# Kernel tuning notes

Hardware: AMD Instinct MI355X
Metric: run time of the kernel (lower is better)

The kernel has to match this reference:

```python
import jax, jax.numpy as jnp
import numpy as np

T, V, D, L, H, F, R = 1024, 17, 1024, 2, 16, 4096, 32
DH = D // H
LORA_SCALE = 2.0  # lora_alpha / r = 64 / 32
MASK_ID = 16
NEG = jnp.float32(-1e9)


def setup_inputs() -> dict:
    key = jax.random.key(0)
    ks = iter(jax.random.split(key, 64))
    def p(shape, std):
        return jax.random.normal(next(ks), shape, jnp.float32) * std
    inp = {
        "packed_context": jax.random.randint(next(ks), (T,), 0, V),
        "cu_seq_lens": jnp.sort(jax.random.randint(next(ks), (5,), 0, T)),
        "max_seq_len": T,
        "row_coords": jax.random.randint(next(ks), (T,), 0, 64),
        "col_coords": jax.random.randint(next(ks), (T,), 0, 64),
        "num_diffusion_steps": 2,
        "E": p((V, D), 0.02),  # embed rows actually used: weight[:vocab_size]
    }
    shapes = {"q": (D, D), "k": (D, D), "v": (D, D), "o": (D, D),
              "g": (D, F), "u": (D, F), "d": (F, D)}
    for nm, (di, do) in shapes.items():
        inp["W" + nm] = p((L, di, do), di ** -0.5)  # frozen NF4 base weight (dequantized)
        inp["A" + nm] = p((L, di, R), di ** -0.5)   # LoRA A
        inp["B" + nm] = p((L, R, do), 0.01)          # LoRA B (nonzero for grad testing)
    inp["ln1"] = jnp.ones((L, D), jnp.float32)
    inp["ln2"] = jnp.ones((L, D), jnp.float32)
    inp["lnf"] = jnp.ones((D,), jnp.float32)
    return inp


def _rms(x, w):
    return x * jax.lax.rsqrt(jnp.mean(x * x, axis=-1, keepdims=True) + 1e-6) * w


def _lora(x, W, A, B):
    # fused base matmul + low-rank LoRA delta
    return x @ W + LORA_SCALE * ((x @ A) @ B)


def _denoise_step(soft, E, Wq, Aq, Bq, Wk, Ak, Bk, Wv, Av, Bv, Wo, Ao, Bo,
                  Wg, Ag, Bg, Wu, Au, Bu, Wd, Ad, Bd, ln1, ln2, lnf, causal_bias):
    # soft-token embedding: [T,V] @ [V,D]
    x = soft @ E
    inv_sqrt_dh = jnp.float32(1.0 / np.sqrt(DH))
    for l in range(L):
        h = _rms(x, ln1[l])
        q = _lora(h, Wq[l], Aq[l], Bq[l]).reshape(T, H, DH)
        k = _lora(h, Wk[l], Ak[l], Bk[l]).reshape(T, H, DH)
        v = _lora(h, Wv[l], Av[l], Bv[l]).reshape(T, H, DH)
        scores = jnp.einsum('qhd,khd->hqk', q, k) * inv_sqrt_dh + causal_bias
        att = jax.nn.softmax(scores, axis=-1)
        ctx = jnp.einsum('hqk,khd->qhd', att, v).reshape(T, D)
        x = x + _lora(ctx, Wo[l], Ao[l], Bo[l])
        h2 = _rms(x, ln2[l])
        ff = jax.nn.silu(_lora(h2, Wg[l], Ag[l], Bg[l])) * _lora(h2, Wu[l], Au[l], Bu[l])
        x = x + _lora(ff, Wd[l], Ad[l], Bd[l])
    logits = _rms(x, lnf) @ E.T  # tied head over the 17-token task vocab
    return jax.nn.softmax(logits, axis=-1)


def reference(packed_context, cu_seq_lens, max_seq_len, row_coords, col_coords,
              num_diffusion_steps, E, Wq, Aq, Bq, Wk, Ak, Bk, Wv, Av, Bv,
              Wo, Ao, Bo, Wg, Ag, Bg, Wu, Au, Bu, Wd, Ad, Bd, ln1, ln2, lnf):
    causal_bias = jnp.where(jnp.tril(jnp.ones((T, T), bool)), jnp.float32(0.0), NEG)
    is_prompt = (packed_context != MASK_ID)[:, None]  # [T,1]
    ctx_onehot = jax.nn.one_hot(packed_context, V, dtype=jnp.float32)
    soft = jnp.zeros((T, V), jnp.float32).at[:, MASK_ID].set(1.0)
    for _ in range(int(num_diffusion_steps)):
        refined = _denoise_step(soft, E, Wq, Aq, Bq, Wk, Ak, Bk, Wv, Av, Bv,
                                Wo, Ao, Bo, Wg, Ag, Bg, Wu, Au, Bu, Wd, Ad, Bd,
                                ln1, ln2, lnf, causal_bias)
        soft = jnp.where(is_prompt, ctx_onehot, refined)
    return jnp.argmax(soft, axis=-1)
```

## Files before the change

### kernel.cpp

```cpp
#include <hip/hip_runtime.h>
#include <hip/hip_bf16.h>

#define T_LEN 1024
#define D_DIM 1024
#define V_DIM 17
#define H_NUM 16
#define DH_DIM 64
#define F_DIM 4096
#define R_LORA 32
#define N_LAYERS 2
#define N_STEPS 2
#define MASK_ID 16
#define LORA_SCALE 2.0f

typedef __attribute__((ext_vector_type(8))) short bfx8;
typedef __attribute__((ext_vector_type(4))) float f32x4;

typedef unsigned short ushort_t;
typedef unsigned int uint_t;

#define AS1 __attribute__((address_space(1)))
#define AS3 __attribute__((address_space(3)))

__device__ __forceinline__ void gload16(const ushort_t* g, ushort_t* l) {
    __builtin_amdgcn_global_load_lds((const AS1 void*)(const void*)g,
                                     (AS3 void*)(void*)l, 16, 0, 0);
}

__device__ __forceinline__ ushort_t f2bf(float v) {
    __hip_bfloat16 h = __float2bfloat16(v);
    return __builtin_bit_cast(unsigned short, h);
}
__device__ __forceinline__ float bf2f(ushort_t u) {
    return __uint_as_float(((uint_t)u) << 16);
}
__device__ __forceinline__ void split4_store(float y0, float y1, float y2, float y3,
                                             ushort_t* __restrict__ hi, ushort_t* __restrict__ lo,
                                             size_t idx) {
    ushort_t h0 = f2bf(y0), h1 = f2bf(y1), h2 = f2bf(y2), h3 = f2bf(y3);
    ushort_t l0 = f2bf(y0 - bf2f(h0));
    ushort_t l1 = f2bf(y1 - bf2f(h1));
    ushort_t l2 = f2bf(y2 - bf2f(h2));
    ushort_t l3 = f2bf(y3 - bf2f(h3));
    uint2 hv, lv;
    hv.x = (uint_t)h0 | ((uint_t)h1 << 16);
    hv.y = (uint_t)h2 | ((uint_t)h3 << 16);
    lv.x = (uint_t)l0 | ((uint_t)l1 << 16);
    lv.y = (uint_t)l2 | ((uint_t)l3 << 16);
    *(uint2*)(hi + idx) = hv;
    *(uint2*)(lo + idx) = lv;
}

__global__ void init_soft_kernel(float* __restrict__ soft) {
    int idx = blockIdx.x * blockDim.x + threadIdx.x;
    if (idx < T_LEN * V_DIM) {
        soft[idx] = ((idx % V_DIM) == MASK_ID) ? 1.0f : 0.0f;
    }
}

__global__ __launch_bounds__(256) void embed_rms_split_kernel(
    const float* __restrict__ soft, const float* __restrict__ E,
    const float* __restrict__ w, float* __restrict__ x,
    ushort_t* __restrict__ hi, ushort_t* __restrict__ lo)
{
    const int t = blockIdx.x, tid = threadIdx.x;
    __shared__ float srow[V_DIM];
    __shared__ float red[4];
    if (tid < V_DIM) srow[tid] = soft[t * V_DIM + tid];
    __syncthreads();
    const int d0 = tid * 4;
    float4 acc = {0.f, 0.f, 0.f, 0.f};
    #pragma unroll
    for (int v = 0; v < V_DIM; v++) {
        float s = srow[v];
        float4 e = *(const float4*)(E + (size_t)v * D_DIM + d0);
        acc.x = fmaf(s, e.x, acc.x);
        acc.y = fmaf(s, e.y, acc.y);
        acc.z = fmaf(s, e.z, acc.z);
        acc.w = fmaf(s, e.w, acc.w);
    }
    size_t base = (size_t)t * D_DIM + d0;
    *(float4*)(x + base) = acc;
    float ss = acc.x * acc.x + acc.y * acc.y + acc.z * acc.z + acc.w * acc.w;
    const int lane = tid & 63, wv = tid >> 6;
    #pragma unroll
    for (int off = 32; off > 0; off >>= 1) ss += __shfl_xor(ss, off);
    if (lane == 0) red[wv] = ss;
    __syncthreads();
    ss = red[0] + red[1] + red[2] + red[3];
    const float r = 1.0f / sqrtf(ss * (1.0f / D_DIM) + 1e-6f);
    const float4 wv4 = *(const float4*)(w + d0);
    split4_store(acc.x * r * wv4.x, acc.y * r * wv4.y, acc.z * r * wv4.z, acc.w * r * wv4.w,
                 hi, lo, base);
}

__global__ __launch_bounds__(256) void fold_kernel(
    const float* __restrict__ W,
    const float* __restrict__ A,
    const float* __restrict__ Bm,
    ushort_t* __restrict__ oHi,
    ushort_t* __restrict__ oLo,
    int K, int N)
{
    const int l = blockIdx.z;
    W   += (size_t)l * K * N;
    A   += (size_t)l * K * R_LORA;
    Bm  += (size_t)l * R_LORA * N;
    oHi += (size_t)l * K * N;
    oLo += (size_t)l * K * N;
    __shared__ float Als[64][R_LORA + 1];
    __shared__ uint_t tile[64][65];
    const int tid = threadIdx.x;
    const int n0 = blockIdx.x * 64, k0 = blockIdx.y * 64;

    {
        const int row = tid >> 2, c0 = (tid & 3) * 8;
        const float* src = A + (size_t)(k0 + row) * R_LORA + c0;
        float4 a0 = *(const float4*)(src);
        float4 a1 = *(const float4*)(src + 4);
        Als[row][c0 + 0] = a0.x; Als[row][c0 + 1] = a0.y;
        Als[row][c0 + 2] = a0.z; Als[row][c0 + 3] = a0.w;
        Als[row][c0 + 4] = a1.x; Als[row][c0 + 5] = a1.y;
        Als[row][c0 + 6] = a1.z; Als[row][c0 + 7] = a1.w;
    }
    const int nl = tid & 63, kq = tid >> 6;
    float wreg[16];
    #pragma unroll
    for (int i = 0; i < 16; i++)
        wreg[i] = W[(size_t)(k0 + kq * 16 + i) * N + n0 + nl];
    float breg[R_LORA];
    #pragma unroll
    for (int r = 0; r < R_LORA; r++) breg[r] = Bm[(size_t)r * N + n0 + nl];
    __syncthreads();
    #pragma unroll
    for (int i = 0; i < 16; i++) {
        const int kl = kq * 16 + i;
        float acc = 0.f;
        #pragma unroll
        for (int r = 0; r < R_LORA; r++) acc = fmaf(Als[kl][r], breg[r], acc);
        float val = wreg[i] + LORA_SCALE * acc;
        ushort_t h = f2bf(val);
        tile[kl][nl] = ((uint_t)h << 16) | (uint_t)f2bf(val - bf2f(h));
    }
    __syncthreads();
    {
        const int nl2 = tid >> 2;
        const int kc0 = (tid & 3) * 16;
        ushort_t hb[16], lb[16];
        #pragma unroll
        for (int i = 0; i < 16; i++) {
            uint_t pk = tile[kc0 + i][nl2];
            hb[i] = (ushort_t)(pk >> 16);
            lb[i] = (ushort_t)(pk & 0xffffu);
        }
        size_t idx = (size_t)(n0 + nl2) * K + k0 + kc0;
        *(uint4*)(oHi + idx)     = *(uint4*)&hb[0];
        *(uint4*)(oHi + idx + 8) = *(uint4*)&hb[8];
        *(uint4*)(oLo + idx)     = *(uint4*)&lb[0];
        *(uint4*)(oLo + idx + 8) = *(uint4*)&lb[8];
    }
}

struct GemmJob {
    const ushort_t* Bh;
    const ushort_t* Bl;
    float* Cf;
    ushort_t* Ch;
    ushort_t* Cl;
    int k0, k1;
};

__global__ __launch_bounds__(256) void gemm128_kernel(
    const ushort_t* __restrict__ Ahi, const ushort_t* __restrict__ Alo,
    int K, int N,
    GemmJob j0, GemmJob j1, GemmJob j2, GemmJob j3,
    GemmJob j4, GemmJob j5, GemmJob j6, GemmJob j7)
{
    GemmJob jb;
    {
        const int z = blockIdx.z;
        if      (z == 0) jb = j0; else if (z == 1) jb = j1;
        else if (z == 2) jb = j2; else if (z == 3) jb = j3;
        else if (z == 4) jb = j4; else if (z == 5) jb = j5;
        else if (z == 6) jb = j6; else jb = j7;
    }
    __shared__ ushort_t Ash[128][32];
    __shared__ ushort_t Asl[128][32];
    __shared__ ushort_t Bsh[128][32];
    __shared__ ushort_t Bsl[128][32];

    const int tid = threadIdx.x, lane = tid & 63, w = tid >> 6;
    const int l15 = lane & 15, lg = lane >> 4;
    const int m0 = blockIdx.y * 128, n0 = blockIdx.x * 128;
    const int wm = (w >> 1) * 64, wn = (w & 1) * 64;

    const int r0 = w * 32;
    const int rsub = lane >> 2;
    const int cs = lane & 3;
    const int csl = (cs ^ ((rsub >> 1) & 3)) * 8;
    const int rsl = (lg ^ ((l15 >> 1) & 3)) * 8;

    f32x4 acc[4][4];
    #pragma unroll
    for (int i = 0; i < 4; i++)
        #pragma unroll
        for (int j = 0; j < 4; j++) acc[i][j] = f32x4{0.f, 0.f, 0.f, 0.f};

    const size_t rowA = (size_t)(m0 + r0 + rsub) * K;
    const size_t rowB = (size_t)(n0 + r0 + rsub) * K;
    const size_t rstep = (size_t)16 * K;

    for (int kk = jb.k0; kk < jb.k1; kk += 32) {
        {
            const ushort_t* a0 = Ahi + rowA + kk + csl;
            const ushort_t* a1 = Alo + rowA + kk + csl;
            const ushort_t* b0 = jb.Bh + rowB + kk + csl;
            const ushort_t* b1 = jb.Bl + rowB + kk + csl;
            gload16(a0,         &Ash[r0][0]);
            gload16(a0 + rstep, &Ash[r0 + 16][0]);
            gload16(a1,         &Asl[r0][0]);
            gload16(a1 + rstep, &Asl[r0 + 16][0]);
            gload16(b0,         &Bsh[r0][0]);
            gload16(b0 + rstep, &Bsh[r0 + 16][0]);
            gload16(b1,         &Bsl[r0][0]);
            gload16(b1 + rstep, &Bsl[r0 + 16][0]);
        }
        __syncthreads();
        bfx8 bh[4], bl[4];
        #pragma unroll
        for (int ni = 0; ni < 4; ni++) {
            bh[ni] = *(const bfx8*)&Bsh[wn + ni * 16 + l15][rsl];
            bl[ni] = *(const bfx8*)&Bsl[wn + ni * 16 + l15][rsl];
        }
        #pragma unroll
        for (int mi = 0; mi < 4; mi++) {
            bfx8 ah = *(const bfx8*)&Ash[wm + mi * 16 + l15][rsl];
            bfx8 al = *(const bfx8*)&Asl[wm + mi * 16 + l15][rsl];
            #pragma unroll
            for (int ni = 0; ni < 4; ni++) {
                acc[mi][ni] = __builtin_amdgcn_mfma_f32_16x16x32_bf16(ah, bh[ni], acc[mi][ni], 0, 0, 0);
                acc[mi][ni] = __builtin_amdgcn_mfma_f32_16x16x32_bf16(ah, bl[ni], acc[mi][ni], 0, 0, 0);
                acc[mi][ni] = __builtin_amdgcn_mfma_f32_16x16x32_bf16(al, bh[ni], acc[mi][ni], 0, 0, 0);
            }
        }
        __syncthreads();
    }

    if (jb.Cf) {
        #pragma unroll
        for (int mi = 0; mi < 4; mi++)
            #pragma unroll
            for (int ni = 0; ni < 4; ni++) {
                int col = n0 + wn + ni * 16 + l15;
                #pragma unroll
                for (int i = 0; i < 4; i++) {
                    int row = m0 + wm + mi * 16 + lg * 4 + i;
                    jb.Cf[(size_t)row * N + col] = acc[mi][ni][i];
                }
            }
    } else {
        #pragma unroll
        for (int mi = 0; mi < 4; mi++)
            #pragma unroll
            for (int ni = 0; ni < 4; ni++) {
                int col = n0 + wn + ni * 16 + l15;
                #pragma unroll
                for (int i = 0; i < 4; i++) {
                    int row = m0 + wm + mi * 16 + lg * 4 + i;
                    size_t idx = (size_t)row * N + col;
                    float v = acc[mi][ni][i];
                    ushort_t h = f2bf(v);
                    jb.Ch[idx] = h;
                    jb.Cl[idx] = f2bf(v - bf2f(h));
                }
            }
    }
}

__global__ __launch_bounds__(256) void qkv2_split_kernel(
    const float* __restrict__ pb,
    ushort_t* __restrict__ qbh, ushort_t* __restrict__ qbl,
    ushort_t* __restrict__ kbh, ushort_t* __restrict__ kbl,
    ushort_t* __restrict__ vbh, ushort_t* __restrict__ vbl)
{
    const size_t DD1 = (size_t)T_LEN * D_DIM;
    size_t e = ((size_t)blockIdx.x * 256 + threadIdx.x) * 4;
    float4 a, b;
    a = *(const float4*)(pb + e);
    b = *(const float4*)(pb + DD1 + e);
    split4_store(a.x + b.x, a.y + b.y, a.z + b.z, a.w + b.w, qbh, qbl, e);
    a = *(const float4*)(pb + 2 * DD1 + e);
    b = *(const float4*)(pb + 3 * DD1 + e);
    split4_store(a.x + b.x, a.y + b.y, a.z + b.z, a.w + b.w, kbh, kbl, e);
    a = *(const float4*)(pb + 4 * DD1 + e);
    b = *(const float4*)(pb + 5 * DD1 + e);
    split4_store(a.x + b.x, a.y + b.y, a.z + b.z, a.w + b.w, vbh, vbl, e);
}

__global__ void add8_kernel(float* __restrict__ x, const float* __restrict__ pb, int n4) {
    int i = blockIdx.x * blockDim.x + threadIdx.x;
    if (i < n4) {
        const size_t DD1 = (size_t)T_LEN * D_DIM;
        size_t e = (size_t)i * 4;
        float4 xv = *(const float4*)(x + e);
        #pragma unroll
        for (int j = 0; j < 8; j++) {
            float4 p = *(const float4*)(pb + j * DD1 + e);
            xv.x += p.x; xv.y += p.y; xv.z += p.z; xv.w += p.w;
        }
        *(float4*)(x + e) = xv;
    }
}

__global__ __launch_bounds__(256) void add8_rms_split_kernel(
    float* __restrict__ x, const float* __restrict__ pb,
    const float* __restrict__ w, ushort_t* __restrict__ hi, ushort_t* __restrict__ lo)
{
    const int t = blockIdx.x, tid = threadIdx.x;
    const size_t DD1 = (size_t)T_LEN * D_DIM;
    size_t base = (size_t)t * D_DIM + tid * 4;
    float4 xv = *(const float4*)(x + base);
    #pragma unroll
    for (int j = 0; j < 8; j++) {
        float4 p = *(const float4*)(pb + j * DD1 + base);
        xv.x += p.x; xv.y += p.y; xv.z += p.z; xv.w += p.w;
    }
    *(float4*)(x + base) = xv;
    float ss = xv.x * xv.x + xv.y * xv.y + xv.z * xv.z + xv.w * xv.w;
    __shared__ float red[4];
    const int lane = tid & 63, wv = tid >> 6;
    #pragma unroll
    for (int off = 32; off > 0; off >>= 1) ss += __shfl_xor(ss, off);
    if (lane == 0) red[wv] = ss;
    __syncthreads();
    ss = red[0] + red[1] + red[2] + red[3];
    const float r = 1.0f / sqrtf(ss * (1.0f / D_DIM) + 1e-6f);
    const float4 wv4 = *(const float4*)(w + tid * 4);
    split4_store(xv.x * r * wv4.x, xv.y * r * wv4.y, xv.z * r * wv4.z, xv.w * r * wv4.w,
                 hi, lo, base);
}

#define KS_PAD 72
#define P_PAD 72
__global__ __launch_bounds__(256, 1) void attn_mfma_kernel(
    const ushort_t* __restrict__ qh, const ushort_t* __restrict__ ql,
    const ushort_t* __restrict__ kh, const ushort_t* __restrict__ kl,
    const ushort_t* __restrict__ vh, const ushort_t* __restrict__ vl,
    ushort_t* __restrict__ chi, ushort_t* __restrict__ clo)
{
    __shared__ ushort_t Ksh[64][KS_PAD];
    __shared__ ushort_t Ksl[64][KS_PAD];
    __shared__ ushort_t VTh[64][KS_PAD];
    __shared__ ushort_t VTl[64][KS_PAD];
    __shared__ ushort_t Ph[4][16][P_PAD];
    __shared__ ushort_t Pl[4][16][P_PAD];

    const int qt = blockIdx.x, hh = blockIdx.y;
    const int tid = threadIdx.x, w = tid >> 6, lane = tid & 63;
    const int l15 = lane & 15, lg = lane >> 4;
    const int q0 = qt * 64;
    const int hcol = hh * DH_DIM;

    bfx8 qa_h[2], qa_l[2];
    {
        size_t qrow = (size_t)(q0 + w * 16 + l15) * D_DIM + hcol;
        #pragma unroll
        for (int ks = 0; ks < 2; ks++) {
            qa_h[ks] = *(const bfx8*)(qh + qrow + ks * 32 + lg * 8);
            qa_l[ks] = *(const bfx8*)(ql + qrow + ks * 32 + lg * 8);
        }
    }

    f32x4 o[4];
    #pragma unroll
    for (int ni = 0; ni < 4; ni++) o[ni] = f32x4{0.f, 0.f, 0.f, 0.f};
    float mrun[4], lrun[4];
    #pragma unroll
    for (int i = 0; i < 4; i++) { mrun[i] = -3.0e38f; lrun[i] = 0.f; }

    const int srow = tid >> 2;
    const int sseg = (tid & 3) * 16;
    const int vp = tid & 31;
    const int vd0 = (tid >> 5) * 8;

    for (int kt = 0; kt <= qt; kt++) {
        __syncthreads();
        {
            size_t src = (size_t)(kt * 64 + srow) * D_DIM + hcol + sseg;
            *(uint4*)&Ksh[srow][sseg]     = *(const uint4*)(kh + src);
            *(uint4*)&Ksh[srow][sseg + 8] = *(const uint4*)(kh + src + 8);
            *(uint4*)&Ksl[srow][sseg]     = *(const uint4*)(kl + src);
            *(uint4*)&Ksl[srow][sseg + 8] = *(const uint4*)(kl + src + 8);
        }
        {
            size_t s0 = (size_t)(kt * 64 + 2 * vp) * D_DIM + hcol + vd0;
            uint4 h0 = *(const uint4*)(vh + s0);
            uint4 h1 = *(const uint4*)(vh + s0 + D_DIM);
            uint4 l0 = *(const uint4*)(vl + s0);
            uint4 l1 = *(const uint4*)(vl + s0 + D_DIM);
            const ushort_t* a = (const ushort_t*)&h0;
            const ushort_t* b = (const ushort_t*)&h1;
            const ushort_t* c = (const ushort_t*)&l0;
            const ushort_t* d = (const ushort_t*)&l1;
            #pragma unroll
            for (int j = 0; j < 8; j++) {
                *(uint_t*)&VTh[vd0 + j][2 * vp] = (uint_t)a[j] | ((uint_t)b[j] << 16);
                *(uint_t*)&VTl[vd0 + j][2 * vp] = (uint_t)c[j] | ((uint_t)d[j] << 16);
            }
        }
        __syncthreads();

        f32x4 s[4];
        #pragma unroll
        for (int ni = 0; ni < 4; ni++) s[ni] = f32x4{0.f, 0.f, 0.f, 0.f};
        #pragma unroll
        for (int ks = 0; ks < 2; ks++) {
            #pragma unroll
            for (int ni = 0; ni < 4; ni++) {
                bfx8 bh = *(const bfx8*)&Ksh[ni * 16 + l15][ks * 32 + lg * 8];
                bfx8 bl = *(const bfx8*)&Ksl[ni * 16 + l15][ks * 32 + lg * 8];
                s[ni] = __builtin_amdgcn_mfma_f32_16x16x32_bf16(qa_h[ks], bh, s[ni], 0, 0, 0);
                s[ni] = __builtin_amdgcn_mfma_f32_16x16x32_bf16(qa_h[ks], bl, s[ni], 0, 0, 0);
                s[ni] = __builtin_amdgcn_mfma_f32_16x16x32_bf16(qa_l[ks], bh, s[ni], 0, 0, 0);
            }
        }

        const int kbase = kt * 64;
        float rmax[4];
        #pragma unroll
        for (int i = 0; i < 4; i++) rmax[i] = -3.0e38f;
        #pragma unroll
        for (int ni = 0; ni < 4; ni++) {
            int kc = kbase + ni * 16 + l15;
            #pragma unroll
            for (int i = 0; i < 4; i++) {
                int qrow = q0 + w * 16 + lg * 4 + i;
                float v = s[ni][i] * 0.125f;
                v = (kc <= qrow) ? v : -3.0e38f;
                s[ni][i] = v;
                rmax[i] = fmaxf(rmax[i], v);
            }
        }
        #pragma unroll
        for (int off = 1; off < 16; off <<= 1) {
            #pragma unroll
            for (int i = 0; i < 4; i++) rmax[i] = fmaxf(rmax[i], __shfl_xor(rmax[i], off));
        }
        float psum[4];
        #pragma unroll
        for (int i = 0; i < 4; i++) {
            float nm = fmaxf(mrun[i], rmax[i]);
            float sc = __expf(mrun[i] - nm);
            lrun[i] *= sc;
            #pragma unroll
            for (int ni = 0; ni < 4; ni++) o[ni][i] *= sc;
            mrun[i] = nm;
            psum[i] = 0.f;
        }
        #pragma unroll
        for (int ni = 0; ni < 4; ni++) {
            #pragma unroll
            for (int i = 0; i < 4; i++) {
                float e = __expf(s[ni][i] - mrun[i]);
                s[ni][i] = e;
                psum[i] += e;
            }
        }
        #pragma unroll
        for (int off = 1; off < 16; off <<= 1) {
            #pragma unroll
            for (int i = 0; i < 4; i++) psum[i] += __shfl_xor(psum[i], off);
        }
        #pragma unroll
        for (int i = 0; i < 4; i++) lrun[i] += psum[i];

        #pragma unroll
        for (int ni = 0; ni < 4; ni++) {
            #pragma unroll
            for (int i = 0; i < 4; i++) {
                float e = s[ni][i];
                ushort_t hp = f2bf(e);
                Ph[w][lg * 4 + i][ni * 16 + l15] = hp;
                Pl[w][lg * 4 + i][ni * 16 + l15] = f2bf(e - bf2f(hp));
            }
        }
        #pragma unroll
        for (int ks = 0; ks < 2; ks++) {
            bfx8 ah = *(const bfx8*)&Ph[w][l15][ks * 32 + lg * 8];
            bfx8 al = *(const bfx8*)&Pl[w][l15][ks * 32 + lg * 8];
            #pragma unroll
            for (int ni = 0; ni < 4; ni++) {
                bfx8 bh = *(const bfx8*)&VTh[ni * 16 + l15][ks * 32 + lg * 8];
                bfx8 bl = *(const bfx8*)&VTl[ni * 16 + l15][ks * 32 + lg * 8];
                o[ni] = __builtin_amdgcn_mfma_f32_16x16x32_bf16(ah, bh, o[ni], 0, 0, 0);
                o[ni] = __builtin_amdgcn_mfma_f32_16x16x32_bf16(ah, bl, o[ni], 0, 0, 0);
                o[ni] = __builtin_amdgcn_mfma_f32_16x16x32_bf16(al, bh, o[ni], 0, 0, 0);
            }
        }
    }

    #pragma unroll
    for (int i = 0; i < 4; i++) {
        float inv = 1.0f / lrun[i];
        #pragma unroll
        for (int ni = 0; ni < 4; ni++) o[ni][i] *= inv;
    }
    #pragma unroll
    for (int ni = 0; ni < 4; ni++) {
        int col = hcol + ni * 16 + l15;
        #pragma unroll
        for (int i = 0; i < 4; i++) {
            int row = q0 + w * 16 + lg * 4 + i;
            size_t idx = (size_t)row * D_DIM + col;
            float v = o[ni][i];
            ushort_t hp = f2bf(v);
            chi[idx] = hp;
            clo[idx] = f2bf(v - bf2f(hp));
        }
    }
}

__global__ void silu_split_kernel(const float* __restrict__ g, const float* __restrict__ u,
                                  ushort_t* __restrict__ hi, ushort_t* __restrict__ lo, int n4) {
    int i = blockIdx.x * blockDim.x + threadIdx.x;
    if (i < n4) {
        float4 gv = *(const float4*)(g + (size_t)i * 4);
        float4 uv = *(const float4*)(u + (size_t)i * 4);
        float y0 = gv.x / (1.f + expf(-gv.x)) * uv.x;
        float y1 = gv.y / (1.f + expf(-gv.y)) * uv.y;
        float y2 = gv.z / (1.f + expf(-gv.z)) * uv.z;
        float y3 = gv.w / (1.f + expf(-gv.w)) * uv.w;
        split4_store(y0, y1, y2, y3, hi, lo, (size_t)i * 4);
    }
}

__global__ __launch_bounds__(256) void head_kernel(const float* __restrict__ x,
                                                   const float* __restrict__ lnf,
                                                   const float* __restrict__ E,
                                                   const int* __restrict__ tok,
                                                   float* __restrict__ soft) {
    int t = blockIdx.x;
    int tid = threadIdx.x;
    __shared__ float y[D_DIM];
    __shared__ float red[4];
    __shared__ float logits[V_DIM];
    const float* xr = x + (size_t)t * D_DIM;
    float ss = 0.f;
    for (int d = tid; d < D_DIM; d += 256) { float v = xr[d]; ss += v * v; }
    int lane = tid & 63, wave = tid >> 6;
    for (int off = 32; off > 0; off >>= 1) ss += __shfl_xor(ss, off);
    if (lane == 0) red[wave] = ss;
    __syncthreads();
    ss = red[0] + red[1] + red[2] + red[3];
    float r = 1.0f / sqrtf(ss * (1.0f / D_DIM) + 1e-6f);
    for (int d = tid; d < D_DIM; d += 256) y[d] = xr[d] * r * lnf[d];
    __syncthreads();
    for (int vv = wave; vv < V_DIM; vv += 4) {
        float p = 0.f;
        for (int d = lane; d < D_DIM; d += 64) p += y[d] * E[vv * D_DIM + d];
        for (int off = 32; off > 0; off >>= 1) p += __shfl_xor(p, off);
        if (lane == 0) logits[vv] = p;
    }
    __syncthreads();
    if (tid == 0) {
        int tk = tok[t];
        if (tk != MASK_ID) {
            for (int vv = 0; vv < V_DIM; vv++) soft[t * V_DIM + vv] = (vv == tk) ? 1.f : 0.f;
        } else {
            float mx = -1e30f;
            for (int vv = 0; vv < V_DIM; vv++) mx = fmaxf(mx, logits[vv]);
            float sm = 0.f;
            float e[V_DIM];
            for (int vv = 0; vv < V_DIM; vv++) { e[vv] = expf(logits[vv] - mx); sm += e[vv]; }
            float invs = 1.0f / sm;
            for (int vv = 0; vv < V_DIM; vv++) soft[t * V_DIM + vv] = e[vv] * invs;
        }
    }
}

__global__ void argmax_kernel(const float* __restrict__ soft, int* __restrict__ out) {
    int t = blockIdx.x * blockDim.x + threadIdx.x;
    if (t < T_LEN) {
        const float* s = soft + t * V_DIM;
        int best = 0;
        float bv = s[0];
        #pragma unroll
        for (int vv = 1; vv < V_DIM; vv++) {
            float v = s[vv];
            if (v > bv) { bv = v; best = vv; }
        }
        out[t] = best;
    }
}

__global__ __launch_bounds__(256) void rms_kernel(const float* __restrict__ x,
                                                  const float* __restrict__ w,
                                                  float* __restrict__ out) {
    int t = blockIdx.x;
    const float* xr = x + (size_t)t * D_DIM;
    float ss = 0.f;
    for (int d = threadIdx.x; d < D_DIM; d += 256) { float v = xr[d]; ss += v * v; }
    __shared__ float red[4];
    int lane = threadIdx.x & 63, wave = threadIdx.x >> 6;
    for (int off = 32; off > 0; off >>= 1) ss += __shfl_xor(ss, off);
    if (lane == 0) red[wave] = ss;
    __syncthreads();
    ss = red[0] + red[1] + red[2] + red[3];
    float r = 1.0f / sqrtf(ss * (1.0f / D_DIM) + 1e-6f);
    for (int d = threadIdx.x; d < D_DIM; d += 256) out[(size_t)t * D_DIM + d] = xr[d] * r * w[d];
}

__global__ __launch_bounds__(256) void embed_kernel(const float* __restrict__ soft,
                                                    const float* __restrict__ E,
                                                    float* __restrict__ x) {
    int t = blockIdx.x;
    __shared__ float srow[V_DIM];
    if (threadIdx.x < V_DIM) srow[threadIdx.x] = soft[t * V_DIM + threadIdx.x];
    __syncthreads();
    for (int d = threadIdx.x; d < D_DIM; d += 256) {
        float acc = 0.f;
        #pragma unroll
        for (int v = 0; v < V_DIM; v++) acc += srow[v] * E[v * D_DIM + d];
        x[(size_t)t * D_DIM + d] = acc;
    }
}

__global__ __launch_bounds__(256) void gemm_kernel(const float* __restrict__ A,
                                                   const float* __restrict__ B,
                                                   float* __restrict__ C,
                                                   int M, int N, int K,
                                                   float alpha, int accumulate) {
    const int BM = 64, BN = 64, BK = 16;
    __shared__ float As[BK][BM];
    __shared__ float Bsh[BK][BN];
    int tid = threadIdx.x;
    int tx = tid % 16, ty = tid / 16;
    int row0 = blockIdx.y * BM, col0 = blockIdx.x * BN;
    float acc[4][4] = {};
    for (int k0 = 0; k0 < K; k0 += BK) {
        #pragma unroll
        for (int i = 0; i < 4; i++) {
            int e = tid * 4 + i;
            int m = e / BK, kk = e % BK;
            int gr = row0 + m, gk = k0 + kk;
            As[kk][m] = (gr < M && gk < K) ? A[(size_t)gr * K + gk] : 0.f;
        }
        #pragma unroll
        for (int i = 0; i < 4; i++) {
            int e = tid * 4 + i;
            int kk = e / BN, n = e % BN;
            int gk = k0 + kk, gc = col0 + n;
            Bsh[kk][n] = (gk < K && gc < N) ? B[(size_t)gk * N + gc] : 0.f;
        }
        __syncthreads();
        #pragma unroll
        for (int kk = 0; kk < BK; kk++) {
            float a[4], b[4];
            #pragma unroll
            for (int i = 0; i < 4; i++) a[i] = As[kk][ty * 4 + i];
            #pragma unroll
            for (int j = 0; j < 4; j++) b[j] = Bsh[kk][tx * 4 + j];
            #pragma unroll
            for (int i = 0; i < 4; i++)
                #pragma unroll
                for (int j = 0; j < 4; j++)
                    acc[i][j] += a[i] * b[j];
        }
        __syncthreads();
    }
    #pragma unroll
    for (int i = 0; i < 4; i++) {
        int r = row0 + ty * 4 + i;
        if (r >= M) continue;
        #pragma unroll
        for (int j = 0; j < 4; j++) {
            int c = col0 + tx * 4 + j;
            if (c >= N) continue;
            size_t idx = (size_t)r * N + c;
            float val = alpha * acc[i][j];
            if (accumulate) val += C[idx];
            C[idx] = val;
        }
    }
}

__global__ __launch_bounds__(256) void attn_kernel(const float* __restrict__ q,
                                                   const float* __restrict__ k,
                                                   const float* __restrict__ v,
                                                   float* __restrict__ ctx) {
    int qi = blockIdx.x;
    int hh = blockIdx.y;
    __shared__ float sc[T_LEN];
    __shared__ float qrow[DH_DIM];
    __shared__ float red[8];
    __shared__ float part[4][DH_DIM];
    int tid = threadIdx.x;
    int lane = tid & 63, wave = tid >> 6;
    const float* qp = q + (size_t)qi * D_DIM + hh * DH_DIM;
    if (tid < DH_DIM) qrow[tid] = qp[tid];
    __syncthreads();
    const float scale = 0.125f;
    for (int j = wave; j <= qi; j += 4) {
        const float* kp = k + (size_t)j * D_DIM + hh * DH_DIM;
        float p = qrow[lane] * kp[lane];
        for (int off = 32; off > 0; off >>= 1) p += __shfl_xor(p, off);
        if (lane == 0) sc[j] = p * scale;
    }
    __syncthreads();
    int n = qi + 1;
    float m = -1e30f;
    for (int j = tid; j < n; j += 256) m = fmaxf(m, sc[j]);
    for (int off = 32; off > 0; off >>= 1) m = fmaxf(m, __shfl_xor(m, off));
    if (lane == 0) red[wave] = m;
    __syncthreads();
    m = fmaxf(fmaxf(red[0], red[1]), fmaxf(red[2], red[3]));
    float s = 0.f;
    for (int j = tid; j < n; j += 256) { float e = expf(sc[j] - m); sc[j] = e; s += e; }
    for (int off = 32; off > 0; off >>= 1) s += __shfl_xor(s, off);
    if (lane == 0) red[4 + wave] = s;
    __syncthreads();
    s = red[4] + red[5] + red[6] + red[7];
    float inv = 1.0f / s;
    float acc = 0.f;
    for (int j = wave; j < n; j += 4) {
        acc += sc[j] * v[(size_t)j * D_DIM + hh * DH_DIM + lane];
    }
    part[wave][lane] = acc;
    __syncthreads();
    if (tid < DH_DIM) {
        float r = (part[0][tid] + part[1][tid] + part[2][tid] + part[3][tid]) * inv;
        ctx[(size_t)qi * D_DIM + hh * DH_DIM + tid] = r;
    }
}

__global__ void silu_mul_kernel(const float* __restrict__ g, const float* __restrict__ u,
                                float* __restrict__ out, int nelem) {
    int i = blockIdx.x * blockDim.x + threadIdx.x;
    if (i < nelem) {
        float gv = g[i];
        float sg = 1.0f / (1.0f + expf(-gv));
        out[i] = gv * sg * u[i];
    }
}

static inline void launch_gemm(const float* A, const float* B, float* C,
                               int M, int N, int K, float alpha, int accumulate,
                               hipStream_t stream) {
    dim3 grid((N + 63) / 64, (M + 63) / 64);
    gemm_kernel<<<grid, 256, 0, stream>>>(A, B, C, M, N, K, alpha, accumulate);
}

extern "C" void kernel_launch(void* const* d_in, const int* in_sizes, int n_in,
                              void* d_out, int out_size, void* d_ws, size_t ws_size,
                              hipStream_t stream) {
    const int* packed = (const int*)d_in[0];
    const float* E  = (const float*)d_in[6];
    const float* Wsrc[7] = {(const float*)d_in[7],  (const float*)d_in[10], (const float*)d_in[13],
                            (const float*)d_in[16], (const float*)d_in[19], (const float*)d_in[22],
                            (const float*)d_in[25]};
    const float* Asrc[7] = {(const float*)d_in[8],  (const float*)d_in[11], (const float*)d_in[14],
                            (const float*)d_in[17], (const float*)d_in[20], (const float*)d_in[23],
                            (const float*)d_in[26]};
    const float* Bsrc[7] = {(const float*)d_in[9],  (const float*)d_in[12], (const float*)d_in[15],
                            (const float*)d_in[18], (const float*)d_in[21], (const float*)d_in[24],
                            (const float*)d_in[27]};
    const float* ln1 = (const float*)d_in[28];
    const float* ln2 = (const float*)d_in[29];
    const float* lnf = (const float*)d_in[30];

    const size_t DD = (size_t)D_DIM * D_DIM;
    const size_t DF = (size_t)D_DIM * F_DIM;
    const size_t wsizes[7] = {DD, DD, DD, DD, DF, DF, DF};
    const int Kdim[7] = {D_DIM, D_DIM, D_DIM, D_DIM, D_DIM, D_DIM, F_DIM};
    const int Ndim[7] = {D_DIM, D_DIM, D_DIM, D_DIM, F_DIM, F_DIM, D_DIM};

    size_t u16_elems = 0;
    for (int p = 0; p < 7; p++) u16_elems += 2ull * N_LAYERS * wsizes[p];
    u16_elems += 2ull * DD;
    u16_elems += 2ull * DD;
    u16_elems += 2ull * DF;
    u16_elems += 6ull * DD;
    size_t f32_elems = (size_t)T_LEN * V_DIM + DD  + 2 * DF ;
    size_t need = u16_elems * 2 + f32_elems * 4 + 256;

    if (ws_size >= need) {
        ushort_t* ub = (ushort_t*)d_ws;
        size_t uo = 0;
        ushort_t *Whi[7], *Wlo[7];
        for (int p = 0; p < 7; p++) {
            Whi[p] = ub + uo; uo += (size_t)N_LAYERS * wsizes[p];
            Wlo[p] = ub + uo; uo += (size_t)N_LAYERS * wsizes[p];
        }
        ushort_t* h_hi = ub + uo; uo += DD;
        ushort_t* h_lo = ub + uo; uo += DD;
        ushort_t* c_hi = ub + uo; uo += DD;
        ushort_t* c_lo = ub + uo; uo += DD;
        ushort_t* f_hi = ub + uo; uo += DF;
        ushort_t* f_lo = ub + uo; uo += DF;
        ushort_t* qbh = ub + uo; uo += DD;
        ushort_t* qbl = ub + uo; uo += DD;
        ushort_t* kbh = ub + uo; uo += DD;
        ushort_t* kbl = ub + uo; uo += DD;
        ushort_t* vbh = ub + uo; uo += DD;
        ushort_t* vbl = ub + uo; uo += DD;
        float* fb = (float*)(ub + uo);
        size_t fo = 0;
        float* soft = fb + fo; fo += (size_t)T_LEN * V_DIM;
        float* x    = fb + fo; fo += DD;
        float* gbuf = fb + fo; fo += DF;
        float* ubuf = fb + fo; fo += DF;
        float* pbase = gbuf;

        for (int p = 0; p < 7; p++) {
            dim3 grid(Ndim[p] / 64, Kdim[p] / 64, N_LAYERS);
            fold_kernel<<<grid, 256, 0, stream>>>(Wsrc[p], Asrc[p], Bsrc[p],
                                                  Whi[p], Wlo[p], Kdim[p], Ndim[p]);
        }

        init_soft_kernel<<<(T_LEN * V_DIM + 255) / 256, 256, 0, stream>>>(soft);

        const int n4 = (int)(DD / 4);
        for (int step = 0; step < N_STEPS; step++) {
            embed_rms_split_kernel<<<T_LEN, 256, 0, stream>>>(soft, E, ln1, x, h_hi, h_lo);
            for (int l = 0; l < N_LAYERS; l++) {
                {
                    GemmJob jq0 = {Whi[0] + l * DD, Wlo[0] + l * DD, pbase + 0 * DD, nullptr, nullptr, 0, 512};
                    GemmJob jq1 = {Whi[0] + l * DD, Wlo[0] + l * DD, pbase + 1 * DD, nullptr, nullptr, 512, 1024};
                    GemmJob jk0 = {Whi[1] + l * DD, Wlo[1] + l * DD, pbase + 2 * DD, nullptr, nullptr, 0, 512};
                    GemmJob jk1 = {Whi[1] + l * DD, Wlo[1] + l * DD, pbase + 3 * DD, nullptr, nullptr, 512, 1024};
                    GemmJob jv0 = {Whi[2] + l * DD, Wlo[2] + l * DD, pbase + 4 * DD, nullptr, nullptr, 0, 512};
                    GemmJob jv1 = {Whi[2] + l * DD, Wlo[2] + l * DD, pbase + 5 * DD, nullptr, nullptr, 512, 1024};
                    gemm128_kernel<<<dim3(8, 8, 6), 256, 0, stream>>>(
                        h_hi, h_lo, D_DIM, D_DIM, jq0, jq1, jk0, jk1, jv0, jv1, jq0, jq0);
                    qkv2_split_kernel<<<(int)(DD / 4 / 256), 256, 0, stream>>>(
                        pbase, qbh, qbl, kbh, kbl, vbh, vbl);
                }
                attn_mfma_kernel<<<dim3(T_LEN / 64, H_NUM), 256, 0, stream>>>(
                    qbh, qbl, kbh, kbl, vbh, vbl, c_hi, c_lo);
                {
                    const ushort_t* bh = Whi[3] + l * DD;
                    const ushort_t* bl = Wlo[3] + l * DD;
                    GemmJob j[8];
                    for (int i = 0; i < 8; i++)
                        j[i] = {bh, bl, pbase + i * DD, nullptr, nullptr, i * 128, (i + 1) * 128};
                    gemm128_kernel<<<dim3(8, 8, 8), 256, 0, stream>>>(
                        c_hi, c_lo, D_DIM, D_DIM, j[0], j[1], j[2], j[3], j[4], j[5], j[6], j[7]);
                    add8_rms_split_kernel<<<T_LEN, 256, 0, stream>>>(
                        x, pbase, ln2 + (size_t)l * D_DIM, h_hi, h_lo);
                }
                {
                    GemmJob jg = {Whi[4] + l * DF, Wlo[4] + l * DF, gbuf, nullptr, nullptr, 0, D_DIM};
                    GemmJob ju = {Whi[5] + l * DF, Wlo[5] + l * DF, ubuf, nullptr, nullptr, 0, D_DIM};
                    gemm128_kernel<<<dim3(32, 8, 2), 256, 0, stream>>>(
                        h_hi, h_lo, D_DIM, F_DIM, jg, ju, jg, jg, jg, jg, jg, jg);
                }
                silu_split_kernel<<<(T_LEN * F_DIM / 4 + 255) / 256, 256, 0, stream>>>(
                    gbuf, ubuf, f_hi, f_lo, T_LEN * F_DIM / 4);
                {
                    const ushort_t* bh = Whi[6] + l * DF;
                    const ushort_t* bl = Wlo[6] + l * DF;
                    GemmJob j[8];
                    for (int i = 0; i < 8; i++)
                        j[i] = {bh, bl, pbase + i * DD, nullptr, nullptr, i * 512, (i + 1) * 512};
                    gemm128_kernel<<<dim3(8, 8, 8), 256, 0, stream>>>(
                        f_hi, f_lo, F_DIM, D_DIM, j[0], j[1], j[2], j[3], j[4], j[5], j[6], j[7]);
                    if (l + 1 < N_LAYERS) {
                        add8_rms_split_kernel<<<T_LEN, 256, 0, stream>>>(
                            x, pbase, ln1 + (size_t)(l + 1) * D_DIM, h_hi, h_lo);
                    } else {
                        add8_kernel<<<(n4 + 255) / 256, 256, 0, stream>>>(x, pbase, n4);
                    }
                }
            }
            head_kernel<<<T_LEN, 256, 0, stream>>>(x, lnf, E, packed, soft);
        }
        argmax_kernel<<<(T_LEN + 255) / 256, 256, 0, stream>>>(soft, (int*)d_out);
        return;
    }

    float* ws = (float*)d_ws;
    size_t off = 0;
    float* soft = ws + off; off += (size_t)T_LEN * V_DIM;
    float* x    = ws + off; off += (size_t)T_LEN * D_DIM;
    float* h    = ws + off; off += (size_t)T_LEN * D_DIM;
    float* qb   = ws + off; off += (size_t)T_LEN * D_DIM;
    float* kb   = ws + off; off += (size_t)T_LEN * D_DIM;
    float* vb   = ws + off; off += (size_t)T_LEN * D_DIM;
    float* cb   = ws + off; off += (size_t)T_LEN * D_DIM;
    float* gb   = ws + off; off += (size_t)T_LEN * F_DIM;
    float* ubf  = ws + off; off += (size_t)T_LEN * F_DIM;
    float* tmp  = ws + off; off += (size_t)T_LEN * R_LORA;

    init_soft_kernel<<<(T_LEN * V_DIM + 255) / 256, 256, 0, stream>>>(soft);
    for (int step = 0; step < N_STEPS; step++) {
        embed_kernel<<<T_LEN, 256, 0, stream>>>(soft, E, x);
        for (int l = 0; l < N_LAYERS; l++) {
            const float* ln1_l = ln1 + (size_t)l * D_DIM;
            const float* ln2_l = ln2 + (size_t)l * D_DIM;
            rms_kernel<<<T_LEN, 256, 0, stream>>>(x, ln1_l, h);
            launch_gemm(h, Asrc[0] + (size_t)l * D_DIM * R_LORA, tmp, T_LEN, R_LORA, D_DIM, 1.0f, 0, stream);
            launch_gemm(h, Wsrc[0] + (size_t)l * DD, qb, T_LEN, D_DIM, D_DIM, 1.0f, 0, stream);
            launch_gemm(tmp, Bsrc[0] + (size_t)l * R_LORA * D_DIM, qb, T_LEN, D_DIM, R_LORA, LORA_SCALE, 1, stream);
            launch_gemm(h, Asrc[1] + (size_t)l * D_DIM * R_LORA, tmp, T_LEN, R_LORA, D_DIM, 1.0f, 0, stream);
            launch_gemm(h, Wsrc[1] + (size_t)l * DD, kb, T_LEN, D_DIM, D_DIM, 1.0f, 0, stream);
            launch_gemm(tmp, Bsrc[1] + (size_t)l * R_LORA * D_DIM, kb, T_LEN, D_DIM, R_LORA, LORA_SCALE, 1, stream);
            launch_gemm(h, Asrc[2] + (size_t)l * D_DIM * R_LORA, tmp, T_LEN, R_LORA, D_DIM, 1.0f, 0, stream);
            launch_gemm(h, Wsrc[2] + (size_t)l * DD, vb, T_LEN, D_DIM, D_DIM, 1.0f, 0, stream);
            launch_gemm(tmp, Bsrc[2] + (size_t)l * R_LORA * D_DIM, vb, T_LEN, D_DIM, R_LORA, LORA_SCALE, 1, stream);
            attn_kernel<<<dim3(T_LEN, H_NUM), 256, 0, stream>>>(qb, kb, vb, cb);
            launch_gemm(cb, Asrc[3] + (size_t)l * D_DIM * R_LORA, tmp, T_LEN, R_LORA, D_DIM, 1.0f, 0, stream);
            launch_gemm(cb, Wsrc[3] + (size_t)l * DD, x, T_LEN, D_DIM, D_DIM, 1.0f, 1, stream);
            launch_gemm(tmp, Bsrc[3] + (size_t)l * R_LORA * D_DIM, x, T_LEN, D_DIM, R_LORA, LORA_SCALE, 1, stream);
            rms_kernel<<<T_LEN, 256, 0, stream>>>(x, ln2_l, h);
            launch_gemm(h, Asrc[4] + (size_t)l * D_DIM * R_LORA, tmp, T_LEN, R_LORA, D_DIM, 1.0f, 0, stream);
            launch_gemm(h, Wsrc[4] + (size_t)l * DF, gb, T_LEN, F_DIM, D_DIM, 1.0f, 0, stream);
            launch_gemm(tmp, Bsrc[4] + (size_t)l * R_LORA * F_DIM, gb, T_LEN, F_DIM, R_LORA, LORA_SCALE, 1, stream);
            launch_gemm(h, Asrc[5] + (size_t)l * D_DIM * R_LORA, tmp, T_LEN, R_LORA, D_DIM, 1.0f, 0, stream);
            launch_gemm(h, Wsrc[5] + (size_t)l * DF, ubf, T_LEN, F_DIM, D_DIM, 1.0f, 0, stream);
            launch_gemm(tmp, Bsrc[5] + (size_t)l * R_LORA * F_DIM, ubf, T_LEN, F_DIM, R_LORA, LORA_SCALE, 1, stream);
            silu_mul_kernel<<<(T_LEN * F_DIM + 255) / 256, 256, 0, stream>>>(gb, ubf, gb, T_LEN * F_DIM);
            launch_gemm(gb, Asrc[6] + (size_t)l * F_DIM * R_LORA, tmp, T_LEN, R_LORA, F_DIM, 1.0f, 0, stream);
            launch_gemm(gb, Wsrc[6] + (size_t)l * DF, x, T_LEN, D_DIM, F_DIM, 1.0f, 1, stream);
            launch_gemm(tmp, Bsrc[6] + (size_t)l * R_LORA * D_DIM, x, T_LEN, D_DIM, R_LORA, LORA_SCALE, 1, stream);
        }
        head_kernel<<<T_LEN, 256, 0, stream>>>(x, lnf, E, packed, soft);
    }
    argmax_kernel<<<(T_LEN + 255) / 256, 256, 0, stream>>>(soft, (int*)d_out);
}
```

Measured before the change: 1.083 ms.

## Generalize split-K GEMM slicing and add deeper split-K when workspace allows

The GEMM kernel gains a kslices parameter so each job is split along K into partial-sum buffers, replacing the hand-built per-slice job lists. With a larger workspace, QKV uses 4 slices, down-projection 16, and gate/up 2 slices, where gate/up previously had none. Silu now sums the gate/up partials itself. The aim is more workgroups per launch to fill the CUs, at the cost of extra partial-buffer memory traffic in the reduction kernels.

```diff
diff --git a/kernel.cpp b/kernel.cpp
--- a/kernel.cpp
+++ b/kernel.cpp
@@ -172,18 +172,26 @@
 
 __global__ __launch_bounds__(256) void gemm128_kernel(
     const ushort_t* __restrict__ Ahi, const ushort_t* __restrict__ Alo,
-    int K, int N,
+    int K, int N, int kslices,
     GemmJob j0, GemmJob j1, GemmJob j2, GemmJob j3,
     GemmJob j4, GemmJob j5, GemmJob j6, GemmJob j7)
 {
     GemmJob jb;
+    int s;
     {
         const int z = blockIdx.z;
-        if      (z == 0) jb = j0; else if (z == 1) jb = j1;
-        else if (z == 2) jb = j2; else if (z == 3) jb = j3;
-        else if (z == 4) jb = j4; else if (z == 5) jb = j5;
-        else if (z == 6) jb = j6; else jb = j7;
-    }
+        const int ji = z / kslices;
+        s = z - ji * kslices;
+        if      (ji == 0) jb = j0; else if (ji == 1) jb = j1;
+        else if (ji == 2) jb = j2; else if (ji == 3) jb = j3;
+        else if (ji == 4) jb = j4; else if (ji == 5) jb = j5;
+        else if (ji == 6) jb = j6; else jb = j7;
+    }
+    const int klen = (jb.k1 - jb.k0) / kslices;
+    const int myk0 = jb.k0 + s * klen;
+    const int myk1 = myk0 + klen;
+    float* Cf = jb.Cf ? jb.Cf + (size_t)s * T_LEN * (size_t)N : nullptr;
+
     __shared__ ushort_t Ash[128][32];
     __shared__ ushort_t Asl[128][32];
     __shared__ ushort_t Bsh[128][32];
@@ -210,7 +218,7 @@
     const size_t rowB = (size_t)(n0 + r0 + rsub) * K;
     const size_t rstep = (size_t)16 * K;
 
-    for (int kk = jb.k0; kk < jb.k1; kk += 32) {
+    for (int kk = myk0; kk < myk1; kk += 32) {
         {
             const ushort_t* a0 = Ahi + rowA + kk + csl;
             const ushort_t* a1 = Alo + rowA + kk + csl;
@@ -246,7 +254,7 @@
         __syncthreads();
     }
 
-    if (jb.Cf) {
+    if (Cf) {
         #pragma unroll
         for (int mi = 0; mi < 4; mi++)
             #pragma unroll
@@ -255,7 +263,7 @@
                 #pragma unroll
                 for (int i = 0; i < 4; i++) {
                     int row = m0 + wm + mi * 16 + lg * 4 + i;
-                    jb.Cf[(size_t)row * N + col] = acc[mi][ni][i];
+                    Cf[(size_t)row * N + col] = acc[mi][ni][i];
                 }
             }
     } else {
@@ -277,52 +285,53 @@
     }
 }
 
-__global__ __launch_bounds__(256) void qkv2_split_kernel(
-    const float* __restrict__ pb,
+__global__ __launch_bounds__(256) void qkv_sum_split_kernel(
+    const float* __restrict__ P, int S,
     ushort_t* __restrict__ qbh, ushort_t* __restrict__ qbl,
     ushort_t* __restrict__ kbh, ushort_t* __restrict__ kbl,
     ushort_t* __restrict__ vbh, ushort_t* __restrict__ vbl)
 {
     const size_t DD1 = (size_t)T_LEN * D_DIM;
     size_t e = ((size_t)blockIdx.x * 256 + threadIdx.x) * 4;
-    float4 a, b;
-    a = *(const float4*)(pb + e);
-    b = *(const float4*)(pb + DD1 + e);
-    split4_store(a.x + b.x, a.y + b.y, a.z + b.z, a.w + b.w, qbh, qbl, e);
-    a = *(const float4*)(pb + 2 * DD1 + e);
-    b = *(const float4*)(pb + 3 * DD1 + e);
-    split4_store(a.x + b.x, a.y + b.y, a.z + b.z, a.w + b.w, kbh, kbl, e);
-    a = *(const float4*)(pb + 4 * DD1 + e);
-    b = *(const float4*)(pb + 5 * DD1 + e);
-    split4_store(a.x + b.x, a.y + b.y, a.z + b.z, a.w + b.w, vbh, vbl, e);
-}
-
-__global__ void add8_kernel(float* __restrict__ x, const float* __restrict__ pb, int n4) {
+    float4 q = {0,0,0,0}, k = {0,0,0,0}, v = {0,0,0,0};
+    for (int j = 0; j < S; j++) {
+        float4 a = *(const float4*)(P + (size_t)j * DD1 + e);
+        q.x += a.x; q.y += a.y; q.z += a.z; q.w += a.w;
+        float4 b = *(const float4*)(P + (size_t)(S + j) * DD1 + e);
+        k.x += b.x; k.y += b.y; k.z += b.z; k.w += b.w;
+        float4 c = *(const float4*)(P + (size_t)(2 * S + j) * DD1 + e);
+        v.x += c.x; v.y += c.y; v.z += c.z; v.w += c.w;
+    }
+    split4_store(q.x, q.y, q.z, q.w, qbh, qbl, e);
+    split4_store(k.x, k.y, k.z, k.w, kbh, kbl, e);
+    split4_store(v.x, v.y, v.z, v.w, vbh, vbl, e);
+}
+
+__global__ void addn_kernel(float* __restrict__ x, const float* __restrict__ P,
+                            int nparts, int n4) {
     int i = blockIdx.x * blockDim.x + threadIdx.x;
     if (i < n4) {
         const size_t DD1 = (size_t)T_LEN * D_DIM;
         size_t e = (size_t)i * 4;
         float4 xv = *(const float4*)(x + e);
-        #pragma unroll
-        for (int j = 0; j < 8; j++) {
-            float4 p = *(const float4*)(pb + j * DD1 + e);
+        for (int j = 0; j < nparts; j++) {
+            float4 p = *(const float4*)(P + (size_t)j * DD1 + e);
             xv.x += p.x; xv.y += p.y; xv.z += p.z; xv.w += p.w;
         }
         *(float4*)(x + e) = xv;
     }
 }
 
-__global__ __launch_bounds__(256) void add8_rms_split_kernel(
-    float* __restrict__ x, const float* __restrict__ pb,
+__global__ __launch_bounds__(256) void add_rms_split_kernel(
+    float* __restrict__ x, const float* __restrict__ P, int nparts,
     const float* __restrict__ w, ushort_t* __restrict__ hi, ushort_t* __restrict__ lo)
 {
     const int t = blockIdx.x, tid = threadIdx.x;
     const size_t DD1 = (size_t)T_LEN * D_DIM;
     size_t base = (size_t)t * D_DIM + tid * 4;
     float4 xv = *(const float4*)(x + base);
-    #pragma unroll
-    for (int j = 0; j < 8; j++) {
-        float4 p = *(const float4*)(pb + j * DD1 + base);
+    for (int j = 0; j < nparts; j++) {
+        float4 p = *(const float4*)(P + (size_t)j * DD1 + base);
         xv.x += p.x; xv.y += p.y; xv.z += p.z; xv.w += p.w;
     }
     *(float4*)(x + base) = xv;
@@ -338,6 +347,24 @@
     const float4 wv4 = *(const float4*)(w + tid * 4);
     split4_store(xv.x * r * wv4.x, xv.y * r * wv4.y, xv.z * r * wv4.z, xv.w * r * wv4.w,
                  hi, lo, base);
+}
+
+__global__ void silu_sum_split_kernel(const float* __restrict__ P, int parts,
+                                      ushort_t* __restrict__ hi, ushort_t* __restrict__ lo) {
+    const size_t DF1 = (size_t)T_LEN * F_DIM;
+    size_t e = ((size_t)blockIdx.x * 256 + threadIdx.x) * 4;
+    float4 g = {0,0,0,0}, u = {0,0,0,0};
+    for (int j = 0; j < parts; j++) {
+        float4 a = *(const float4*)(P + (size_t)j * DF1 + e);
+        g.x += a.x; g.y += a.y; g.z += a.z; g.w += a.w;
+        float4 b = *(const float4*)(P + (size_t)(parts + j) * DF1 + e);
+        u.x += b.x; u.y += b.y; u.z += b.z; u.w += b.w;
+    }
+    float y0 = g.x / (1.f + expf(-g.x)) * u.x;
+    float y1 = g.y / (1.f + expf(-g.y)) * u.y;
+    float y2 = g.z / (1.f + expf(-g.z)) * u.z;
+    float y3 = g.w / (1.f + expf(-g.w)) * u.w;
+    split4_store(y0, y1, y2, y3, hi, lo, e);
 }
 
 #define KS_PAD 72
@@ -517,20 +544,6 @@
             chi[idx] = hp;
             clo[idx] = f2bf(v - bf2f(hp));
         }
-    }
-}
-
-__global__ void silu_split_kernel(const float* __restrict__ g, const float* __restrict__ u,
-                                  ushort_t* __restrict__ hi, ushort_t* __restrict__ lo, int n4) {
-    int i = blockIdx.x * blockDim.x + threadIdx.x;
-    if (i < n4) {
-        float4 gv = *(const float4*)(g + (size_t)i * 4);
-        float4 uv = *(const float4*)(u + (size_t)i * 4);
-        float y0 = gv.x / (1.f + expf(-gv.x)) * uv.x;
-        float y1 = gv.y / (1.f + expf(-gv.y)) * uv.y;
-        float y2 = gv.z / (1.f + expf(-gv.z)) * uv.z;
-        float y3 = gv.w / (1.f + expf(-gv.w)) * uv.w;
-        split4_store(y0, y1, y2, y3, hi, lo, (size_t)i * 4);
     }
 }
 
@@ -780,10 +793,13 @@
     u16_elems += 2ull * DD;
     u16_elems += 2ull * DF;
     u16_elems += 6ull * DD;
-    size_t f32_elems = (size_t)T_LEN * V_DIM + DD  + 2 * DF ;
-    size_t need = u16_elems * 2 + f32_elems * 4 + 256;
-
-    if (ws_size >= need) {
+    size_t f32_mid = (size_t)T_LEN * V_DIM + DD + 8 * DD;
+    size_t f32_big = (size_t)T_LEN * V_DIM + DD + 16 * DD;
+    size_t need_mid = u16_elems * 2 + f32_mid * 4 + 256;
+    size_t need_big = u16_elems * 2 + f32_big * 4 + 256;
+
+    if (ws_size >= need_mid) {
+        const bool big = (ws_size >= need_big);
         ushort_t* ub = (ushort_t*)d_ws;
         size_t uo = 0;
         ushort_t *Whi[7], *Wlo[7];
@@ -807,9 +823,7 @@
         size_t fo = 0;
         float* soft = fb + fo; fo += (size_t)T_LEN * V_DIM;
         float* x    = fb + fo; fo += DD;
-        float* gbuf = fb + fo; fo += DF;
-        float* ubuf = fb + fo; fo += DF;
-        float* pbase = gbuf;
+        float* P    = fb + fo;
 
         for (int p = 0; p < 7; p++) {
             dim3 grid(Ndim[p] / 64, Kdim[p] / 64, N_LAYERS);
@@ -820,55 +834,49 @@
         init_soft_kernel<<<(T_LEN * V_DIM + 255) / 256, 256, 0, stream>>>(soft);
 
         const int n4 = (int)(DD / 4);
+        const int qkvS = big ? 4 : 2;
+        const int dprS = big ? 16 : 8;
+        const int guS  = big ? 2 : 1;
+        GemmJob jz = {};
+
         for (int step = 0; step < N_STEPS; step++) {
             embed_rms_split_kernel<<<T_LEN, 256, 0, stream>>>(soft, E, ln1, x, h_hi, h_lo);
             for (int l = 0; l < N_LAYERS; l++) {
                 {
-                    GemmJob jq0 = {Whi[0] + l * DD, Wlo[0] + l * DD, pbase + 0 * DD, nullptr, nullptr, 0, 512};
-                    GemmJob jq1 = {Whi[0] + l * DD, Wlo[0] + l * DD, pbase + 1 * DD, nullptr, nullptr, 512, 1024};
-                    GemmJob jk0 = {Whi[1] + l * DD, Wlo[1] + l * DD, pbase + 2 * DD, nullptr, nullptr, 0, 512};
-                    GemmJob jk1 = {Whi[1] + l * DD, Wlo[1] + l * DD, pbase + 3 * DD, nullptr, nullptr, 512, 1024};
-                    GemmJob jv0 = {Whi[2] + l * DD, Wlo[2] + l * DD, pbase + 4 * DD, nullptr, nullptr, 0, 512};
-                    GemmJob jv1 = {Whi[2] + l * DD, Wlo[2] + l * DD, pbase + 5 * DD, nullptr, nullptr, 512, 1024};
-                    gemm128_kernel<<<dim3(8, 8, 6), 256, 0, stream>>>(
-                        h_hi, h_lo, D_DIM, D_DIM, jq0, jq1, jk0, jk1, jv0, jv1, jq0, jq0);
-                    qkv2_split_kernel<<<(int)(DD / 4 / 256), 256, 0, stream>>>(
-                        pbase, qbh, qbl, kbh, kbl, vbh, vbl);
+                    GemmJob jq = {Whi[0] + l * DD, Wlo[0] + l * DD, P,                      nullptr, nullptr, 0, D_DIM};
+                    GemmJob jk = {Whi[1] + l * DD, Wlo[1] + l * DD, P + (size_t)qkvS * DD,  nullptr, nullptr, 0, D_DIM};
+                    GemmJob jv = {Whi[2] + l * DD, Wlo[2] + l * DD, P + (size_t)2 * qkvS * DD, nullptr, nullptr, 0, D_DIM};
+                    gemm128_kernel<<<dim3(8, 8, 3 * qkvS), 256, 0, stream>>>(
+                        h_hi, h_lo, D_DIM, D_DIM, qkvS, jq, jk, jv, jz, jz, jz, jz, jz);
+                    qkv_sum_split_kernel<<<(int)(DD / 4 / 256), 256, 0, stream>>>(
+                        P, qkvS, qbh, qbl, kbh, kbl, vbh, vbl);
                 }
                 attn_mfma_kernel<<<dim3(T_LEN / 64, H_NUM), 256, 0, stream>>>(
                     qbh, qbl, kbh, kbl, vbh, vbl, c_hi, c_lo);
                 {
-                    const ushort_t* bh = Whi[3] + l * DD;
-                    const ushort_t* bl = Wlo[3] + l * DD;
-                    GemmJob j[8];
-                    for (int i = 0; i < 8; i++)
-                        j[i] = {bh, bl, pbase + i * DD, nullptr, nullptr, i * 128, (i + 1) * 128};
+                    GemmJob jo = {Whi[3] + l * DD, Wlo[3] + l * DD, P, nullptr, nullptr, 0, D_DIM};
                     gemm128_kernel<<<dim3(8, 8, 8), 256, 0, stream>>>(
-                        c_hi, c_lo, D_DIM, D_DIM, j[0], j[1], j[2], j[3], j[4], j[5], j[6], j[7]);
-                    add8_rms_split_kernel<<<T_LEN, 256, 0, stream>>>(
-                        x, pbase, ln2 + (size_t)l * D_DIM, h_hi, h_lo);
+                        c_hi, c_lo, D_DIM, D_DIM, 8, jo, jz, jz, jz, jz, jz, jz, jz);
+                    add_rms_split_kernel<<<T_LEN, 256, 0, stream>>>(
+                        x, P, 8, ln2 + (size_t)l * D_DIM, h_hi, h_lo);
                 }
                 {
-                    GemmJob jg = {Whi[4] + l * DF, Wlo[4] + l * DF, gbuf, nullptr, nullptr, 0, D_DIM};
-                    GemmJob ju = {Whi[5] + l * DF, Wlo[5] + l * DF, ubuf, nullptr, nullptr, 0, D_DIM};
-                    gemm128_kernel<<<dim3(32, 8, 2), 256, 0, stream>>>(
-                        h_hi, h_lo, D_DIM, F_DIM, jg, ju, jg, jg, jg, jg, jg, jg);
+                    GemmJob jg = {Whi[4] + l * DF, Wlo[4] + l * DF, P,                     nullptr, nullptr, 0, D_DIM};
+                    GemmJob ju = {Whi[5] + l * DF, Wlo[5] + l * DF, P + (size_t)guS * DF,  nullptr, nullptr, 0, D_DIM};
+                    gemm128_kernel<<<dim3(32, 8, 2 * guS), 256, 0, stream>>>(
+                        h_hi, h_lo, D_DIM, F_DIM, guS, jg, ju, jz, jz, jz, jz, jz, jz);
+                    silu_sum_split_kernel<<<(int)(DF / 4 / 256), 256, 0, stream>>>(
+                        P, guS, f_hi, f_lo);
                 }
-                silu_split_kernel<<<(T_LEN * F_DIM / 4 + 255) / 256, 256, 0, stream>>>(
-                    gbuf, ubuf, f_hi, f_lo, T_LEN * F_DIM / 4);
                 {
-                    const ushort_t* bh = Whi[6] + l * DF;
-                    const ushort_t* bl = Wlo[6] + l * DF;
-                    GemmJob j[8];
-                    for (int i = 0; i < 8; i++)
-                        j[i] = {bh, bl, pbase + i * DD, nullptr, nullptr, i * 512, (i + 1) * 512};
-                    gemm128_kernel<<<dim3(8, 8, 8), 256, 0, stream>>>(
-                        f_hi, f_lo, F_DIM, D_DIM, j[0], j[1], j[2], j[3], j[4], j[5], j[6], j[7]);
+                    GemmJob jd = {Whi[6] + l * DF, Wlo[6] + l * DF, P, nullptr, nullptr, 0, F_DIM};
+                    gemm128_kernel<<<dim3(8, 8, dprS), 256, 0, stream>>>(
+                        f_hi, f_lo, F_DIM, D_DIM, dprS, jd, jz, jz, jz, jz, jz, jz, jz);
                     if (l + 1 < N_LAYERS) {
-                        add8_rms_split_kernel<<<T_LEN, 256, 0, stream>>>(
-                            x, pbase, ln1 + (size_t)(l + 1) * D_DIM, h_hi, h_lo);
+                        add_rms_split_kernel<<<T_LEN, 256, 0, stream>>>(
+                            x, P, dprS, ln1 + (size_t)(l + 1) * D_DIM, h_hi, h_lo);
                     } else {
-                        add8_kernel<<<(n4 + 255) / 256, 256, 0, stream>>>(x, pbase, n4);
+                        addn_kernel<<<(n4 + 255) / 256, 256, 0, stream>>>(x, P, dprS, n4);
                     }
                 }
             }
```

Measured after the change: 1.201 ms. +10.9%, slower.
